# Performance work log

Measured on AMD Instinct MI355X. Metric: run time of the kernel, lower is better.

## Reference

```python
import jax, jax.numpy as jnp
import numpy as np

B, S, D, H, E, K = 4, 2048, 1024, 4096, 8, 2

def setup_inputs() -> dict:
    key = jax.random.key(0)
    ks = jax.random.split(key, 7)
    scale = 0.02
    return {
        "x": jax.random.normal(ks[0], (B, S, D), dtype=jnp.float32),
        "Wg": jax.random.normal(ks[1], (D, E), dtype=jnp.float32) * scale,
        "bg": jnp.zeros((E,), dtype=jnp.float32),
        "W1": jax.random.normal(ks[2], (E, D, H), dtype=jnp.float32) * scale,
        "b1": jnp.zeros((E, H), dtype=jnp.float32),
        "W2": jax.random.normal(ks[3], (E, H, D), dtype=jnp.float32) * scale,
        "b2": jnp.zeros((E, D), dtype=jnp.float32),
    }

def reference(x, Wg, bg, W1, b1, W2, b2):
    # Gate: top-k over expert logits, softmax over the k selected logits
    logits = jnp.einsum("bsd,de->bse", x, Wg) + bg          # [B,S,E]
    topv, topi = jax.lax.top_k(logits, K)                     # [B,S,K]
    w = jax.nn.softmax(topv, axis=-1)                          # [B,S,K]
    # Combine weights per expert: sum_k w_k * one_hot(idx_k)
    combine = jnp.sum(jax.nn.one_hot(topi, E, dtype=x.dtype) * w[..., None], axis=-2)  # [B,S,E]
    # Dense per-expert FFN weighted by combine weight (zero weight -> no contribution,
    # identical math to the original masked gather/scatter formulation).
    out = jnp.zeros_like(x)
    for e in range(E):
        h = jax.nn.gelu(jnp.einsum("bsd,dh->bsh", x, W1[e]) + b1[e], approximate=False)
        y = jnp.einsum("bsh,hd->bsd", h, W2[e]) + b2[e]
        out = out + combine[..., e:e + 1] * y
    return out
```

## Files before the change

### kernel.cpp

```cpp
#include <hip/hip_runtime.h>
#include <math.h>

#define TOK   8192
#define DDIM  1024
#define HDIM  4096
#define NEXP  8
#define CAP   17408
#define NMT   136
#define BM    128
#define BN    128
#define BK    32

typedef __attribute__((ext_vector_type(8))) short  bfrag;
typedef __attribute__((ext_vector_type(4))) float  ffrag;
typedef __attribute__((ext_vector_type(8))) unsigned short us8;

__device__ __forceinline__ unsigned short f2bf(float f) {
  unsigned int u = __float_as_uint(f);
  u = (u + 0x7FFFu + ((u >> 16) & 1u)) >> 16;
  return (unsigned short)u;
}
__device__ __forceinline__ float bf2f(unsigned short u) {
  return __uint_as_float((unsigned int)u << 16);
}

__device__ __forceinline__ void gll16(const void* g, void* l) {
  __builtin_amdgcn_global_load_lds(
      (const __attribute__((address_space(1))) unsigned int*)g,
      (__attribute__((address_space(3))) unsigned int*)l,
      16, 0, 0);
}

__global__ __launch_bounds__(256) void transpose_v5(const float* __restrict__ W1,
                                                    unsigned short* __restrict__ w1b,
                                                    const float* __restrict__ W2,
                                                    unsigned short* __restrict__ w2b) {
  int orig = blockIdx.x;
  int bid = (orig & 7) * 256 + (orig >> 3);
  const float* in; unsigned short* out; int R, C, tile;
  if (bid < 1024) { in = W1; out = w1b; R = DDIM; C = HDIM; tile = bid; }
  else            { in = W2; out = w2b; R = HDIM; C = DDIM; tile = bid - 1024; }
  int e = tile >> 7;
  int t = tile & 127;
  int tpr = C >> 8;
  int ty = t / tpr, tx = t % tpr;
  size_t bo = (size_t)e * R * C;
  in += bo; out += bo;
  int r0 = ty * 128, c0 = tx * 256;

  __shared__ __align__(16) float T[64 * 68];
  int tid = threadIdx.x;
  int r4 = (tid >> 4) * 4;
  int c4 = (tid & 15) * 4;
  int oc = tid >> 2;
  int kg = (tid & 3) * 16;

  auto ld = [&](int s, float4* v) {
    int rb = r0 + (s >> 2) * 64;
    int cb = c0 + (s & 3) * 64;
    v[0] = *(const float4*)&in[(size_t)(rb + r4 + 0) * C + cb + c4];
    v[1] = *(const float4*)&in[(size_t)(rb + r4 + 1) * C + cb + c4];
    v[2] = *(const float4*)&in[(size_t)(rb + r4 + 2) * C + cb + c4];
    v[3] = *(const float4*)&in[(size_t)(rb + r4 + 3) * C + cb + c4];
  };

  float4 v[4], nv[4];
  ld(0, v);
#pragma unroll
  for (int s = 0; s < 8; ++s) {
    if (s + 1 < 8) ld(s + 1, nv);
    int rb = r0 + (s >> 2) * 64;
    int cb = c0 + (s & 3) * 64;
    float4 t0 = { v[0].x, v[1].x, v[2].x, v[3].x };
    float4 t1 = { v[0].y, v[1].y, v[2].y, v[3].y };
    float4 t2 = { v[0].z, v[1].z, v[2].z, v[3].z };
    float4 t3 = { v[0].w, v[1].w, v[2].w, v[3].w };
    *(float4*)&T[(c4 + 0) * 68 + r4] = t0;
    *(float4*)&T[(c4 + 1) * 68 + r4] = t1;
    *(float4*)&T[(c4 + 2) * 68 + r4] = t2;
    *(float4*)&T[(c4 + 3) * 68 + r4] = t3;
    __syncthreads();
    float4 f0 = *(const float4*)&T[oc * 68 + kg + 0];
    float4 f1 = *(const float4*)&T[oc * 68 + kg + 4];
    float4 f2 = *(const float4*)&T[oc * 68 + kg + 8];
    float4 f3 = *(const float4*)&T[oc * 68 + kg + 12];
    us8 a, b;
    a[0] = (short)f2bf(f0.x); a[1] = (short)f2bf(f0.y);
    a[2] = (short)f2bf(f0.z); a[3] = (short)f2bf(f0.w);
    a[4] = (short)f2bf(f1.x); a[5] = (short)f2bf(f1.y);
    a[6] = (short)f2bf(f1.z); a[7] = (short)f2bf(f1.w);
    b[0] = (short)f2bf(f2.x); b[1] = (short)f2bf(f2.y);
    b[2] = (short)f2bf(f2.z); b[3] = (short)f2bf(f2.w);
    b[4] = (short)f2bf(f3.x); b[5] = (short)f2bf(f3.y);
    b[6] = (short)f2bf(f3.z); b[7] = (short)f2bf(f3.w);
    size_t sub = ((size_t)(cb >> 6) * (R >> 6) + (rb >> 6)) * 4096;
    *(us8*)&out[sub + oc * 64 + kg + 0] = a;
    *(us8*)&out[sub + oc * 64 + kg + 8] = b;
    __syncthreads();
    v[0] = nv[0]; v[1] = nv[1]; v[2] = nv[2]; v[3] = nv[3];
  }
}

__global__ __launch_bounds__(256) void gate_v3(const float* __restrict__ x,
                                               const float* __restrict__ Wg,
                                               const float* __restrict__ bg,
                                               unsigned short* __restrict__ xb,
                                               int* __restrict__ topi,
                                               float* __restrict__ topw,
                                               int* __restrict__ cnt,
                                               int* __restrict__ token_of) {
  __shared__ int hist[NEXP];
  int tid = threadIdx.x;
  if (tid < NEXP) hist[tid] = 0;
  int gid = blockIdx.x * 256 + tid;
  if (gid < CAP) token_of[gid] = -1;
  __syncthreads();

  int w = tid >> 6, l = tid & 63;
  const float4* wg4 = (const float4*)Wg;
#pragma unroll 1
  for (int ti = 0; ti < 8; ++ti) {
    int t = (blockIdx.x * 4 + w) * 8 + ti;
    const float4* xr = (const float4*)(x + (size_t)t * DDIM);
    float acc[8];
#pragma unroll
    for (int e = 0; e < 8; ++e) acc[e] = 0.f;
#pragma unroll
    for (int gi = 0; gi < 2; ++gi) {
      int f = gi * 128 + 2 * l;
      float4 a0 = xr[f], a1 = xr[f + 1];
      us8 o;
      o[0] = (short)f2bf(a0.x); o[1] = (short)f2bf(a0.y);
      o[2] = (short)f2bf(a0.z); o[3] = (short)f2bf(a0.w);
      o[4] = (short)f2bf(a1.x); o[5] = (short)f2bf(a1.y);
      o[6] = (short)f2bf(a1.z); o[7] = (short)f2bf(a1.w);
      *(us8*)&xb[(size_t)t * DDIM + f * 4] = o;
      float xs[8] = { a0.x, a0.y, a0.z, a0.w, a1.x, a1.y, a1.z, a1.w };
      int dbase = f * 4;
#pragma unroll
      for (int c = 0; c < 8; ++c) {
        float4 w0 = wg4[(dbase + c) * 2 + 0];
        float4 w1 = wg4[(dbase + c) * 2 + 1];
        acc[0] += xs[c] * w0.x; acc[1] += xs[c] * w0.y;
        acc[2] += xs[c] * w0.z; acc[3] += xs[c] * w0.w;
        acc[4] += xs[c] * w1.x; acc[5] += xs[c] * w1.y;
        acc[6] += xs[c] * w1.z; acc[7] += xs[c] * w1.w;
      }
    }
#pragma unroll
    for (int off = 32; off >= 1; off >>= 1)
#pragma unroll
      for (int e = 0; e < 8; ++e) acc[e] += __shfl_down(acc[e], off);
    if (l == 0) {
      float v[8];
#pragma unroll
      for (int e = 0; e < 8; ++e) v[e] = acc[e] + bg[e];
      int i0 = 0;
#pragma unroll
      for (int e = 1; e < 8; ++e) if (v[e] > v[i0]) i0 = e;
      int i1 = -1;
#pragma unroll
      for (int e = 0; e < 8; ++e) if (e != i0 && (i1 < 0 || v[e] > v[i1])) i1 = e;
      float e1 = expf(v[i1] - v[i0]);
      float s = 1.f + e1;
      topi[t * 2 + 0] = i0; topi[t * 2 + 1] = i1;
      topw[t * 2 + 0] = 1.f / s; topw[t * 2 + 1] = e1 / s;
      atomicAdd(&hist[i0], 1);
      atomicAdd(&hist[i1], 1);
    }
  }
  __syncthreads();
  if (tid < NEXP) atomicAdd(&cnt[tid], hist[tid]);
}

__device__ __forceinline__ void local_scan(const int* __restrict__ cnt, int* offs) {
  int o = 0;
#pragma unroll
  for (int e = 0; e < NEXP; ++e) {
    offs[e] = o;
    o += ((cnt[e] + 127) >> 7) << 7;
  }
  offs[NEXP] = o;
}

__global__ __launch_bounds__(256) void assign_kernel(const int* __restrict__ topi,
                                                     const int* __restrict__ cnt,
                                                     int* __restrict__ cursor,
                                                     int* __restrict__ row_of,
                                                     int* __restrict__ token_of) {
  int offs[NEXP + 1];
  local_scan(cnt, offs);
  int id = blockIdx.x * 256 + threadIdx.x;
  if (id >= TOK * 2) return;
  int e = topi[id];
  int slot = atomicAdd(&cursor[e], 1);
  int row = offs[e] + slot;
  row_of[id] = row;
  token_of[row] = id >> 1;
}

template<bool INDIRECT, bool GELU>
__global__ __launch_bounds__(256)
void moe_gemm(const unsigned short* __restrict__ A,
              const unsigned short* __restrict__ B0,
              const float* __restrict__ bias0,
              unsigned short* __restrict__ out,
              int N, int K,
              const int* __restrict__ cnt,
              const int* __restrict__ token_of) {
  int offsets[NEXP + 1];
  local_scan(cnt, offsets);

  int nwg = gridDim.x * gridDim.y;
  int orig = blockIdx.y * gridDim.x + blockIdx.x;
  int V = nwg >> 3;
  int vid = (orig & 7) * V + (orig >> 3);
  int xcd = vid / V;
  int vloc = vid - xcd * V;
  int P = V / gridDim.x;
  int CW = gridDim.x >= 8 ? 8 : gridDim.x;
  int per = P * CW;
  int g = vloc / per;
  int rem = vloc - g * per;
  int m = rem / CW;
  int bx = g * CW + (rem - m * CW);
  int by = xcd * P + m;

  int row0 = by * BM;
  if (row0 >= offsets[NEXP]) return;
  int e = 0;
  while (row0 >= offsets[e + 1]) ++e;
  const unsigned short* B = B0 + (size_t)e * N * K;
  const float* bias = bias0 + (size_t)e * N;
  int n0 = bx * BN;

  __shared__ __align__(16) char sm[49152];

  int tid = threadIdx.x;
  int w = tid >> 6, l = tid & 63;
  int lrow = l & 15, kq = l >> 4;
  int wm = w >> 1, wn = w & 1;

  int c2 = (l & 7) ^ (l >> 3);
  int rloc = ((l >> 3) << 1) + (c2 >> 2);
  int ksw = (c2 & 3) * 16;
  int s0 = 2 * w, s1 = 2 * w + 1;

  int gr0 = row0 + s0 * 16 + rloc, gr1 = row0 + s1 * 16 + rloc;
  int ar0, ar1;
  if (INDIRECT) {
    int t0 = token_of[gr0]; ar0 = t0 < 0 ? 0 : t0;
    int t1 = token_of[gr1]; ar1 = t1 < 0 ? 0 : t1;
  } else { ar0 = gr0; ar1 = gr1; }
  const char* srcA0 = (const char*)(A + (size_t)ar0 * K) + ksw;
  const char* srcA1 = (const char*)(A + (size_t)ar1 * K) + ksw;
  auto bsrc = [&](int nloc) -> const char* {
    int n = n0 + nloc;
    return (const char*)B + ((size_t)(n >> 6) * (K >> 6)) * 8192 + (n & 63) * 128 + ksw;
  };
  const char* srcB0 = bsrc(s0 * 16 + rloc);
  const char* srcB1 = bsrc(s1 * 16 + rloc);

  auto stage = [&](int buf, int k0) {
    int kbA = k0 * 2;
    int kbB = (k0 >> 6) * 8192 + (k0 & 63) * 2;
    gll16(srcA0 + kbA, sm + buf * 8192 + s0 * 1024);
    gll16(srcA1 + kbA, sm + buf * 8192 + s1 * 1024);
    gll16(srcB0 + kbB, sm + 24576 + buf * 8192 + s0 * 1024);
    gll16(srcB1 + kbB, sm + 24576 + buf * 8192 + s1 * 1024);
  };

  int offA[4], offB[4];
#pragma unroll
  for (int i = 0; i < 4; ++i) {
    int ra = wm * 64 + i * 16 + lrow;
    offA[i] = (ra >> 1) * 128 + (((((ra & 1) << 2) + kq) ^ ((ra >> 1) & 7)) << 4);
    int rb = wn * 64 + i * 16 + lrow;
    offB[i] = 24576 + (rb >> 1) * 128 + (((((rb & 1) << 2) + kq) ^ ((rb >> 1) & 7)) << 4);
  }

  ffrag acc[4][4];
#pragma unroll
  for (int i = 0; i < 4; ++i)
#pragma unroll
    for (int j = 0; j < 4; ++j) acc[i][j] = (ffrag){0.f, 0.f, 0.f, 0.f};

  auto compute = [&](int buf) {
    int ab = buf * 8192;
    bfrag a[4], b[4];
#pragma unroll
    for (int i = 0; i < 4; ++i) a[i] = *(const bfrag*)(sm + ab + offA[i]);
#pragma unroll
    for (int j = 0; j < 4; ++j) b[j] = *(const bfrag*)(sm + ab + offB[j]);
#pragma unroll
    for (int i = 0; i < 4; ++i)
#pragma unroll
      for (int j = 0; j < 4; ++j)
        acc[i][j] = __builtin_amdgcn_mfma_f32_16x16x32_bf16(a[i], b[j], acc[i][j], 0, 0, 0);
  };

  stage(0, 0); stage(1, 32);
  asm volatile("s_waitcnt vmcnt(4)" ::: "memory");
  __builtin_amdgcn_s_barrier();

  int nk = K / BK;
  int cur = 0;
  for (int kt = 0; kt < nk; ++kt) {
    int nxt2 = cur + 2; if (nxt2 >= 3) nxt2 -= 3;
    if (kt + 2 < nk) stage(nxt2, (kt + 2) * 32);
    compute(cur);
    if (kt + 1 < nk) {
      if (kt + 2 < nk) { asm volatile("s_waitcnt vmcnt(4)" ::: "memory"); }
      else             { asm volatile("s_waitcnt vmcnt(0)" ::: "memory"); }
    }
    __builtin_amdgcn_s_barrier();
    ++cur; if (cur == 3) cur = 0;
  }

  unsigned short* ht = (unsigned short*)sm;
#pragma unroll
  for (int j = 0; j < 4; ++j) {
    int col = wn * 64 + j * 16 + lrow;
    float bj = bias[n0 + col];
#pragma unroll
    for (int i = 0; i < 4; ++i) {
      int rl = wm * 64 + i * 16 + kq * 4;
#pragma unroll
      for (int r = 0; r < 4; ++r) {
        float v = acc[i][j][r] + bj;
        if (GELU) {
          float z = 1.5957691216f * (v + 0.044715f * v * v * v);
          v = v / (1.0f + __expf(-z));
        }
        ht[(rl + r) * BN + col] = f2bf(v);
      }
    }
  }
  __syncthreads();
#pragma unroll
  for (int it = 0; it < 8; ++it) {
    int c = it * 256 + tid;
    int row = c >> 4;
    int cc = (c & 15) * 8;
    us8 v = *(const us8*)&ht[row * BN + cc];
    *(us8*)&out[(size_t)(row0 + row) * N + n0 + cc] = v;
  }
}

__global__ __launch_bounds__(256) void combine_kernel(const unsigned short* __restrict__ y,
                                                      const int* __restrict__ row_of,
                                                      const float* __restrict__ topw,
                                                      float* __restrict__ out) {
  int t = blockIdx.x;
  int r0 = row_of[t * 2 + 0], r1 = row_of[t * 2 + 1];
  float w0 = topw[t * 2 + 0], w1 = topw[t * 2 + 1];
  const ushort4* y0 = (const ushort4*)(y + (size_t)r0 * DDIM);
  const ushort4* y1 = (const ushort4*)(y + (size_t)r1 * DDIM);
  float4* o = (float4*)(out + (size_t)t * DDIM);
  int i = threadIdx.x;
  ushort4 a = y0[i], b = y1[i];
  float4 r = { w0 * bf2f(a.x) + w1 * bf2f(b.x), w0 * bf2f(a.y) + w1 * bf2f(b.y),
               w0 * bf2f(a.z) + w1 * bf2f(b.z), w0 * bf2f(a.w) + w1 * bf2f(b.w) };
  o[i] = r;
}

extern "C" void kernel_launch(void* const* d_in, const int* in_sizes, int n_in,
                              void* d_out, int out_size, void* d_ws, size_t ws_size,
                              hipStream_t stream) {
  const float* x  = (const float*)d_in[0];
  const float* Wg = (const float*)d_in[1];
  const float* bg = (const float*)d_in[2];
  const float* W1 = (const float*)d_in[3];
  const float* b1 = (const float*)d_in[4];
  const float* W2 = (const float*)d_in[5];
  const float* b2 = (const float*)d_in[6];
  float* out = (float*)d_out;

  size_t off = 0;
  char* base = (char*)d_ws;
  auto alloc = [&](size_t bytes) -> void* {
    void* p = base + off;
    off += (bytes + 255) & ~(size_t)255;
    return p;
  };
  unsigned short* xb  = (unsigned short*)alloc((size_t)TOK * DDIM * 2);
  unsigned short* w1b = (unsigned short*)alloc((size_t)NEXP * HDIM * DDIM * 2);
  unsigned short* w2b = (unsigned short*)alloc((size_t)NEXP * DDIM * HDIM * 2);
  unsigned short* h   = (unsigned short*)alloc((size_t)CAP * HDIM * 2);
  unsigned short* y   = (unsigned short*)alloc((size_t)CAP * DDIM * 2);
  int*   topi     = (int*)alloc((size_t)TOK * 2 * 4);
  float* topw     = (float*)alloc((size_t)TOK * 2 * 4);
  int*   row_of   = (int*)alloc((size_t)TOK * 2 * 4);
  int*   token_of = (int*)alloc((size_t)CAP * 4);
  int*   cntcur   = (int*)alloc(64);
  if (off > ws_size) return;

  int* cnt = cntcur;
  int* cursor = cntcur + 8;

  hipMemsetAsync(cntcur, 0, 64, stream);

  gate_v3<<<256, 256, 0, stream>>>(x, Wg, bg, xb, topi, topw, cnt, token_of);
  transpose_v5<<<2048, 256, 0, stream>>>(W1, w1b, W2, w2b);
  assign_kernel<<<(TOK * 2) / 256, 256, 0, stream>>>(topi, cnt, cursor,
                                                     row_of, token_of);

  moe_gemm<true, true><<<dim3(HDIM / BN, NMT), 256, 0, stream>>>(
      xb, w1b, b1, h, HDIM, DDIM, cnt, token_of);
  moe_gemm<false, false><<<dim3(DDIM / BN, NMT), 256, 0, stream>>>(
      h, w2b, b2, y, DDIM, HDIM, cnt, token_of);

  combine_kernel<<<TOK, 256, 0, stream>>>(y, row_of, topw, out);
}
```

Before: 551.8 us.

## Add 256x256-tile 512-thread kernel for second MoE GEMM with deeper pipelining

Replaces the second expert GEMM (h × W2) with a new kernel that uses 256x256 output tiles, 512 threads, a 128 KB shared-memory double buffer, swizzled LDS reads and interleaved quarter-tile MFMA phases with s_setprio. Expert segments are now padded to multiples of 256 rows (capacity raised) so each tile maps to one expert. The larger tile raises arithmetic intensity and cuts global traffic for the K=4096 GEMM. The cost is higher LDS and register use per block, lower occupancy, and extra padded rows the first GEMM now also processes.

```diff
diff --git a/kernel.cpp b/kernel.cpp
--- a/kernel.cpp
+++ b/kernel.cpp
@@ -5,11 +5,7 @@
 #define DDIM  1024
 #define HDIM  4096
 #define NEXP  8
-#define CAP   17408
-#define NMT   136
-#define BM    128
-#define BN    128
-#define BK    32
+#define CAP   18432
 
 typedef __attribute__((ext_vector_type(8))) short  bfrag;
 typedef __attribute__((ext_vector_type(4))) float  ffrag;
@@ -178,7 +174,7 @@
 #pragma unroll
   for (int e = 0; e < NEXP; ++e) {
     offs[e] = o;
-    o += ((cnt[e] + 127) >> 7) << 7;
+    o += ((cnt[e] + 255) >> 8) << 8;
   }
   offs[NEXP] = o;
 }
@@ -226,13 +222,13 @@
   int bx = g * CW + (rem - m * CW);
   int by = xcd * P + m;
 
-  int row0 = by * BM;
+  int row0 = by * 128;
   if (row0 >= offsets[NEXP]) return;
   int e = 0;
   while (row0 >= offsets[e + 1]) ++e;
   const unsigned short* B = B0 + (size_t)e * N * K;
   const float* bias = bias0 + (size_t)e * N;
-  int n0 = bx * BN;
+  int n0 = bx * 128;
 
   __shared__ __align__(16) char sm[49152];
 
@@ -303,7 +299,7 @@
   asm volatile("s_waitcnt vmcnt(4)" ::: "memory");
   __builtin_amdgcn_s_barrier();
 
-  int nk = K / BK;
+  int nk = K / 32;
   int cur = 0;
   for (int kt = 0; kt < nk; ++kt) {
     int nxt2 = cur + 2; if (nxt2 >= 3) nxt2 -= 3;
@@ -332,7 +328,7 @@
           float z = 1.5957691216f * (v + 0.044715f * v * v * v);
           v = v / (1.0f + __expf(-z));
         }
-        ht[(rl + r) * BN + col] = f2bf(v);
+        ht[(rl + r) * 128 + col] = f2bf(v);
       }
     }
   }
@@ -342,8 +338,158 @@
     int c = it * 256 + tid;
     int row = c >> 4;
     int cc = (c & 15) * 8;
-    us8 v = *(const us8*)&ht[row * BN + cc];
+    us8 v = *(const us8*)&ht[row * 128 + cc];
     *(us8*)&out[(size_t)(row0 + row) * N + n0 + cc] = v;
+  }
+}
+
+__global__ __launch_bounds__(512)
+void moe_gemm2(const unsigned short* __restrict__ A,
+               const unsigned short* __restrict__ B0,
+               const float* __restrict__ bias0,
+               unsigned short* __restrict__ y,
+               const int* __restrict__ cnt) {
+  constexpr int N = DDIM, K = HDIM;
+  int offs[NEXP + 1];
+  local_scan(cnt, offs);
+
+  int nwg = gridDim.x * gridDim.y;
+  int orig = blockIdx.y * gridDim.x + blockIdx.x;
+  int V = nwg >> 3;
+  int vid = (orig & 7) * V + (orig >> 3);
+  int bx = vid & 3, by = vid >> 2;
+
+  int row0 = by * 256;
+  if (row0 >= offs[NEXP]) return;
+  int e = 0;
+  while (row0 >= offs[e + 1]) ++e;
+  const unsigned short* B = B0 + (size_t)e * N * K;
+  const float* bias = bias0 + (size_t)e * N;
+  int n0 = bx * 256;
+
+  __shared__ __align__(16) char sm[131072];
+
+  int tid = threadIdx.x;
+  int w = tid >> 6, l = tid & 63;
+  int lrow = l & 15, kq = l >> 4;
+  int wm = w & 1, wn = w >> 1;
+
+  int cg = (l & 7) ^ (l >> 3);
+
+  const char* sA[2][2];
+  const char* sB[2][2];
+#pragma unroll
+  for (int h2 = 0; h2 < 2; ++h2)
+#pragma unroll
+    for (int j = 0; j < 2; ++j) {
+      int g = row0 + j * 128 + h2 * 64 + w * 8 + (l >> 3);
+      sA[h2][j] = (const char*)A + (size_t)g * (K * 2) + cg * 16;
+      int ntile = bx * 4 + j * 2 + (w >> 2);
+      int nloc = h2 * 32 + (w & 3) * 8 + (l >> 3);
+      sB[h2][j] = (const char*)B + ((size_t)ntile * (K >> 6)) * 8192 + nloc * 128 + cg * 16;
+    }
+
+  auto issueA = [&](int t, int h2) {
+    int dst = (t & 1) * 32768 + h2 * 16384 + w * 1024 + l * 16;
+    int kb = t * 128;
+    gll16(sA[h2][0] + kb, sm + dst);
+    gll16(sA[h2][1] + kb, sm + dst + 8192);
+  };
+  auto issueB = [&](int t, int h2) {
+    int dst = 65536 + (t & 1) * 32768 + h2 * 16384 + w * 1024 + l * 16;
+    int kb = t * 8192;
+    gll16(sB[h2][0] + kb, sm + dst);
+    gll16(sB[h2][1] + kb, sm + dst + 8192);
+  };
+  auto rdA = [&](int bufo, int qm, int i, int ks) -> bfrag {
+    int r = wm * 64 + i * 16 + lrow;
+    int cc = (ks * 4 + kq) ^ (r & 7);
+    return *(const bfrag*)(sm + bufo + qm * 16384 + r * 128 + cc * 16);
+  };
+  auto rdB = [&](int bufo, int qn, int nj, int ks) -> bfrag {
+    int r = wn * 32 + nj * 16 + lrow;
+    int cc = (ks * 4 + kq) ^ (r & 7);
+    return *(const bfrag*)(sm + 65536 + bufo + qn * 16384 + r * 128 + cc * 16);
+  };
+
+  ffrag acc[8][4];
+#pragma unroll
+  for (int i = 0; i < 8; ++i)
+#pragma unroll
+    for (int j = 0; j < 4; ++j) acc[i][j] = (ffrag){0.f, 0.f, 0.f, 0.f};
+
+#define MFMA_Q(MO, NO)                                                           \
+  __builtin_amdgcn_s_setprio(1);                                                 \
+  _Pragma("unroll")                                                              \
+  for (int i = 0; i < 4; ++i)                                                    \
+    _Pragma("unroll")                                                            \
+    for (int nj = 0; nj < 2; ++nj) {                                             \
+      acc[i + MO][nj + NO] = __builtin_amdgcn_mfma_f32_16x16x32_bf16(            \
+          a[i][0], b[nj][0], acc[i + MO][nj + NO], 0, 0, 0);                     \
+      acc[i + MO][nj + NO] = __builtin_amdgcn_mfma_f32_16x16x32_bf16(            \
+          a[i][1], b[nj][1], acc[i + MO][nj + NO], 0, 0, 0);                     \
+    }                                                                            \
+  __builtin_amdgcn_s_setprio(0);
+
+  issueA(0, 0); issueB(0, 0); issueB(0, 1); issueA(0, 1);
+
+  const int NT = K / 64;
+  bfrag a[4][2], b[2][2];
+#pragma unroll 1
+  for (int t = 0; t < NT; ++t) {
+    int bufo = (t & 1) * 32768;
+    bool pre = (t + 1 < NT);
+    asm volatile("s_waitcnt vmcnt(4)" ::: "memory");
+    __builtin_amdgcn_s_barrier();
+#pragma unroll
+    for (int i = 0; i < 4; ++i) { a[i][0] = rdA(bufo, 0, i, 0); a[i][1] = rdA(bufo, 0, i, 1); }
+#pragma unroll
+    for (int nj = 0; nj < 2; ++nj) { b[nj][0] = rdB(bufo, 0, nj, 0); b[nj][1] = rdB(bufo, 0, nj, 1); }
+    if (pre) issueA(t + 1, 0);
+    MFMA_Q(0, 0)
+    if (pre) { asm volatile("s_waitcnt vmcnt(4)" ::: "memory"); }
+    else     { asm volatile("s_waitcnt vmcnt(2)" ::: "memory"); }
+    __builtin_amdgcn_s_barrier();
+#pragma unroll
+    for (int nj = 0; nj < 2; ++nj) { b[nj][0] = rdB(bufo, 1, nj, 0); b[nj][1] = rdB(bufo, 1, nj, 1); }
+    if (pre) issueB(t + 1, 0);
+    MFMA_Q(0, 2)
+    if (pre) { asm volatile("s_waitcnt vmcnt(4)" ::: "memory"); }
+    else     { asm volatile("s_waitcnt vmcnt(0)" ::: "memory"); }
+    __builtin_amdgcn_s_barrier();
+#pragma unroll
+    for (int i = 0; i < 4; ++i) { a[i][0] = rdA(bufo, 1, i, 0); a[i][1] = rdA(bufo, 1, i, 1); }
+    if (pre) issueB(t + 1, 1);
+    MFMA_Q(4, 2)
+    __builtin_amdgcn_s_barrier();
+#pragma unroll
+    for (int nj = 0; nj < 2; ++nj) { b[nj][0] = rdB(bufo, 0, nj, 0); b[nj][1] = rdB(bufo, 0, nj, 1); }
+    if (pre) issueA(t + 1, 1);
+    MFMA_Q(4, 0)
+  }
+#undef MFMA_Q
+
+  __syncthreads();
+  unsigned short* ht = (unsigned short*)sm;
+#pragma unroll
+  for (int mi = 0; mi < 8; ++mi) {
+    int rl = wm * 128 + (mi >> 2) * 64 + (mi & 3) * 16 + kq * 4;
+#pragma unroll
+    for (int nj = 0; nj < 4; ++nj) {
+      int col = wn * 64 + (nj >> 1) * 32 + (nj & 1) * 16 + lrow;
+      float bj = bias[n0 + col];
+#pragma unroll
+      for (int r = 0; r < 4; ++r)
+        ht[(rl + r) * 256 + col] = f2bf(acc[mi][nj][r] + bj);
+    }
+  }
+  __syncthreads();
+#pragma unroll
+  for (int it = 0; it < 16; ++it) {
+    int s = it * 512 + tid;
+    int row = s >> 5, c = (s & 31) * 8;
+    us8 v = *(const us8*)(ht + row * 256 + c);
+    *(us8*)&y[(size_t)(row0 + row) * N + n0 + c] = v;
   }
 }
 
@@ -405,10 +551,10 @@
   assign_kernel<<<(TOK * 2) / 256, 256, 0, stream>>>(topi, cnt, cursor,
                                                      row_of, token_of);
 
-  moe_gemm<true, true><<<dim3(HDIM / BN, NMT), 256, 0, stream>>>(
+  moe_gemm<true, true><<<dim3(HDIM / 128, CAP / 128), 256, 0, stream>>>(
       xb, w1b, b1, h, HDIM, DDIM, cnt, token_of);
-  moe_gemm<false, false><<<dim3(DDIM / BN, NMT), 256, 0, stream>>>(
-      h, w2b, b2, y, DDIM, HDIM, cnt, token_of);
+  moe_gemm2<<<dim3(DDIM / 256, CAP / 256), 512, 0, stream>>>(
+      h, w2b, b2, y, cnt);
 
   combine_kernel<<<TOK, 256, 0, stream>>>(y, row_of, topw, out);
 }
```

Result: slower. 576.0 us (+4.4%).
